# Kernel optimization log

Hardware: AMD Instinct MI355X
Metric: run time of the kernel (lower is better)

## Reference

```python
import jax, jax.numpy as jnp
import numpy as np

EPS = 1e-5  # torch LayerNorm default
H, DH = 8, 64  # heads, dim_head


def _ln(x, g, b):
    mu = jnp.mean(x, axis=-1, keepdims=True)
    var = jnp.var(x, axis=-1, keepdims=True)
    return (x - mu) / jnp.sqrt(var + EPS) * g + b


def setup_inputs() -> dict:
    key = jax.random.key(0)
    ks = jax.random.split(key, 8)
    B, N, M, D, CD = 4, 2048, 256, 1024, 768
    J = M + 1 + N  # context + null + self
    return {
        "x": jax.random.normal(ks[0], (B, N, D), jnp.float32),
        "context": jax.random.normal(ks[1], (B, M, CD), jnp.float32),
        "att_bias": jax.random.normal(ks[2], (B, H, N, J), jnp.float32) * 0.02,
        "ln_g": jnp.ones((D,), jnp.float32),
        "ln_b": jnp.zeros((D,), jnp.float32),
        "null_kv": jax.random.normal(ks[3], (2, DH), jnp.float32),
        "Wq": jax.random.normal(ks[4], (D, H * DH), jnp.float32) * 0.02,
        "Wkv": jax.random.normal(ks[5], (D, 2 * DH), jnp.float32) * 0.02,
        "cln_g": jnp.ones((CD,), jnp.float32),
        "cln_b": jnp.zeros((CD,), jnp.float32),
        "Wc": jax.random.normal(ks[6], (CD, 2 * DH), jnp.float32) * 0.02,
        "bc": jnp.zeros((2 * DH,), jnp.float32),
        "Wo": jax.random.normal(ks[7], (H * DH, D), jnp.float32) * 0.02,
        "oln_g": jnp.ones((D,), jnp.float32),
        "oln_b": jnp.zeros((D,), jnp.float32),
    }


def reference(x, context, att_bias, ln_g, ln_b, null_kv, Wq, Wkv,
              cln_g, cln_b, Wc, bc, Wo, oln_g, oln_b):
    B, N, D = x.shape
    scale = DH ** -0.5
    xn = _ln(x, ln_g, ln_b)
    # queries: per-head [b,h,n,dh], pre-scaled
    q = (xn @ Wq).reshape(B, N, H, DH).transpose(0, 2, 1, 3) * scale
    # shared single-head k/v [b,n,dh]
    kv = xn @ Wkv
    k, v = kv[..., :DH], kv[..., DH:]
    # context k/v [b,m,dh]
    ckv = _ln(context, cln_g, cln_b) @ Wc + bc
    ck, cv = ckv[..., :DH], ckv[..., DH:]
    # null kv token [b,1,dh]
    nk = jnp.broadcast_to(null_kv[0], (B, 1, DH))
    nv = jnp.broadcast_to(null_kv[1], (B, 1, DH))
    # torch order: cat null first, then context -> (ck, nk, k)
    k = jnp.concatenate([ck, nk, k], axis=1)  # [b, j, dh]
    v = jnp.concatenate([cv, nv, v], axis=1)
    score = jnp.einsum('bhid,bjd->bhij', q, k) + att_bias
    probs = jax.nn.softmax(score.astype(jnp.float32), axis=-1).astype(v.dtype)
    att = jnp.einsum('bhij,bjd->bhid', probs, v)
    att = att.transpose(0, 2, 1, 3).reshape(B, N, H * DH)
    return _ln(att @ Wo, oln_g, oln_b)
```

## Files before the change

kernel.cpp:

```cpp
#include <hip/hip_runtime.h>
#include <hip/hip_bf16.h>
#include <cstdint>
#include <cstddef>

#define Bq  4
#define Nq  2048
#define Mq  256
#define Dq  1024
#define CDq 768
#define Hq  8
#define DHq 64
#define Jq  2305
#define QKVN 640
#define NCH 37
#define J2  (NCH * 64)

typedef __bf16  bf16x8 __attribute__((ext_vector_type(8)));
typedef float   f32x4  __attribute__((ext_vector_type(4)));
typedef float   f32x4u __attribute__((ext_vector_type(4), aligned(4)));
typedef float   f32x16 __attribute__((ext_vector_type(16)));
typedef short   s16x8  __attribute__((ext_vector_type(8)));
typedef short   s16x4  __attribute__((ext_vector_type(4)));
typedef unsigned int u32x4 __attribute__((ext_vector_type(4)));
typedef unsigned short u16;
typedef unsigned int   u32;

__device__ __forceinline__ u16 f2b(float v) {
  unsigned x = __builtin_bit_cast(unsigned, v);
  unsigned r = (x + 0x7fffu + ((x >> 16) & 1u)) >> 16;
  return (u16)r;
}
__device__ __forceinline__ float b2f(u16 u) {
  unsigned x = ((unsigned)u) << 16;
  return __builtin_bit_cast(float, x);
}
__device__ __forceinline__ u32 cvtpk(float lo, float hi) {
  u32 r;
  asm("v_cvt_pk_bf16_f32 %0, %1, %2" : "=v"(r) : "v"(lo), "v"(hi));
  return r;
}
__device__ __forceinline__ void pswap(u32& a, u32& b) {
  asm volatile("v_permlane32_swap_b32 %0, %1" : "+v"(a), "+v"(b));
}
__device__ __forceinline__ f32x4 mfma16(bf16x8 a, bf16x8 b, f32x4 c) {
  return __builtin_amdgcn_mfma_f32_16x16x32_bf16(a, b, c, 0, 0, 0);
}
__device__ __forceinline__ f32x16 mfma32(bf16x8 a, bf16x8 b, f32x16 c) {
  return __builtin_amdgcn_mfma_f32_32x32x16_bf16(a, b, c, 0, 0, 0);
}
__device__ __forceinline__ bf16x8 frag_ld(const u16* p) {
  return __builtin_bit_cast(bf16x8, *(const s16x8*)p);
}
__device__ __forceinline__ void stout(float* p, float v) { *p = v; }
__device__ __forceinline__ void stout(u16*   p, float v) { *p = f2b(v); }

__device__ __forceinline__ void gl_lds16(const void* gSrc, void* ldsDst) {
  __builtin_amdgcn_global_load_lds(
      (const __attribute__((address_space(1))) void*)gSrc,
      (__attribute__((address_space(3))) void*)ldsDst, 16, 0, 0);
}

__global__ __launch_bounds__(256) void prep_kernel(
    const float* __restrict__ x,   const float* __restrict__ ln_g,
    const float* __restrict__ ln_b, u16* __restrict__ xn,
    const float* __restrict__ ctx, const float* __restrict__ cln_g,
    const float* __restrict__ cln_b, u16* __restrict__ ctxn,
    const float* __restrict__ Wq, const float* __restrict__ Wkv,
    const float* __restrict__ Wc, const float* __restrict__ Wo,
    u16* __restrict__ WqkvT, u16* __restrict__ WcT, u16* __restrict__ WoT) {
  const int tid = threadIdx.x;
  if (blockIdx.x < Bq * Nq + Bq * Mq) {
    const int row = blockIdx.x;
    const float* in; const float* g; const float* bb; u16* out; int D;
    if (row < Bq * Nq) {
      in = x + (size_t)row * Dq; g = ln_g; bb = ln_b;
      out = xn + (size_t)row * Dq; D = Dq;
    } else {
      int r2 = row - Bq * Nq;
      in = ctx + (size_t)r2 * CDq; g = cln_g; bb = cln_b;
      out = ctxn + (size_t)r2 * CDq; D = CDq;
    }
    __shared__ float buf[1024];
    __shared__ float red[8];
    float s = 0.f, s2 = 0.f;
    for (int i = tid; i < D; i += 256) {
      float v = in[i];
      buf[i] = v;
      s += v; s2 += v * v;
    }
    #pragma unroll
    for (int off = 32; off; off >>= 1) {
      s  += __shfl_down(s,  off);
      s2 += __shfl_down(s2, off);
    }
    if ((tid & 63) == 0) { red[tid >> 6] = s; red[4 + (tid >> 6)] = s2; }
    __syncthreads();
    float sum = red[0] + red[1] + red[2] + red[3];
    float sq  = red[4] + red[5] + red[6] + red[7];
    float mean = sum / D;
    float var  = sq / D - mean * mean;
    float rstd = rsqrtf(var + 1e-5f);
    for (int i = tid; i < D; i += 256)
      out[i] = f2b((buf[i] - mean) * rstd * g[i] + bb[i]);
  } else {
    __shared__ float T[32][33];
    int bid = blockIdx.x - (Bq * Nq + Bq * Mq);
    const float* W; u16* WT; int K, N, bx, by;
    if (bid < 512)      { W = Wq;  WT = WqkvT;                    K = 1024; N = 512;  bx = bid % 16;        by = bid / 16; }
    else if (bid < 640) { W = Wkv; WT = WqkvT + (size_t)512*1024; K = 1024; N = 128;  bx = (bid-512) % 4;   by = (bid-512) / 4; }
    else if (bid < 736) { W = Wc;  WT = WcT;                      K = 768;  N = 128;  bx = (bid-640) % 4;   by = (bid-640) / 4; }
    else                { W = Wo;  WT = WoT;                      K = 512;  N = 1024; bx = (bid-736) % 32;  by = (bid-736) / 32; }
    const int n0 = bx * 32, k0 = by * 32;
    const int tx = tid & 31, ty = tid >> 5;
    #pragma unroll
    for (int i = 0; i < 32; i += 8)
      T[ty + i][tx] = W[(size_t)(k0 + ty + i) * N + n0 + tx];
    __syncthreads();
    #pragma unroll
    for (int i = 0; i < 32; i += 8)
      WT[(size_t)(n0 + ty + i) * K + k0 + tx] = f2b(T[tx][ty + i]);
  }
}

template <typename OT>
__device__ __forceinline__ void gemm_body(const u16* __restrict__ A,
                                          const u16* __restrict__ BT,
                                          OT* __restrict__ C,
                                          int N, int K, int m0, int n0,
                                          u16* Al, u16* Bl) {
  const int tid  = threadIdx.x;
  const int lane = tid & 63, wave = tid >> 6;
  const int l16  = lane & 15, lhi = lane >> 4;
  const int wm = (wave >> 1) * 64, wn = (wave & 1) * 64;

  const int offB = (wave << 10) + (lane << 4);
  const int srow = offB >> 6;
  const int scby = offB & 63;

  f32x4 acc[4][4];
  #pragma unroll
  for (int i = 0; i < 4; ++i)
    #pragma unroll
    for (int j = 0; j < 4; ++j) acc[i][j] = f32x4{0.f, 0.f, 0.f, 0.f};

  for (int k0 = 0; k0 < K; k0 += 32) {
    __syncthreads();
    #pragma unroll
    for (int c = 0; c < 2; ++c) {
      gl_lds16((const char*)(A  + (size_t)(m0 + srow + c * 64) * K + k0) + scby,
               (char*)Al + c * 4096 + (wave << 10));
      gl_lds16((const char*)(BT + (size_t)(n0 + srow + c * 64) * K + k0) + scby,
               (char*)Bl + c * 4096 + (wave << 10));
    }
    __syncthreads();

    bf16x8 af[4], bfr[4];
    #pragma unroll
    for (int mt = 0; mt < 4; ++mt)
      af[mt] = frag_ld(Al + (wm + mt * 16 + l16) * 32 + lhi * 8);
    #pragma unroll
    for (int nt = 0; nt < 4; ++nt)
      bfr[nt] = frag_ld(Bl + (wn + nt * 16 + l16) * 32 + lhi * 8);
    __builtin_amdgcn_s_setprio(1);
    #pragma unroll
    for (int mt = 0; mt < 4; ++mt)
      #pragma unroll
      for (int nt = 0; nt < 4; ++nt)
        acc[mt][nt] = mfma16(af[mt], bfr[nt], acc[mt][nt]);
    __builtin_amdgcn_s_setprio(0);
  }

  #pragma unroll
  for (int mt = 0; mt < 4; ++mt)
    #pragma unroll
    for (int nt = 0; nt < 4; ++nt)
      #pragma unroll
      for (int r = 0; r < 4; ++r)
        stout(C + (size_t)(m0 + wm + mt * 16 + lhi * 4 + r) * N
                + (n0 + wn + nt * 16 + l16),
              acc[mt][nt][r]);
}

__global__ __launch_bounds__(256) void gemm_qkv_ckv(
    const u16* __restrict__ xn, const u16* __restrict__ WqkvT,
    u16* __restrict__ qkv,
    const u16* __restrict__ ctxn, const u16* __restrict__ WcT,
    u16* __restrict__ ckvb) {
  const u16 *A, *BT; u16* C; int N, K, m0, n0;
  if (blockIdx.y < 5) {
    A = xn; BT = WqkvT; C = qkv; N = QKVN; K = Dq;
    m0 = blockIdx.x * 128; n0 = blockIdx.y * 128;
  } else {
    if (blockIdx.x >= 8) return;
    A = ctxn; BT = WcT; C = ckvb; N = 2 * DHq; K = CDq;
    m0 = blockIdx.x * 128; n0 = 0;
  }
  __shared__ __align__(16) u16 Al[128 * 32];
  __shared__ __align__(16) u16 Bl[128 * 32];
  gemm_body<u16>(A, BT, C, N, K, m0, n0, Al, Bl);
}

__global__ void build_kv(const u16* __restrict__ qkv,
                         const u16* __restrict__ ckvb,
                         const float* __restrict__ nullkv,
                         const float* __restrict__ bc,
                         u16* __restrict__ Kt, u16* __restrict__ Vt) {
  int idx = blockIdx.x * 256 + threadIdx.x;
  if (idx >= Bq * J2 * 64) return;
  int d = idx & 63;
  int t = idx >> 6;
  int j = t % J2;
  int b = t / J2;
  float k = 0.f, v = 0.f;
  if (j < Mq) {
    const u16* p = ckvb + (size_t)(b * Mq + j) * 128;
    k = b2f(p[d])      + bc[d];
    v = b2f(p[64 + d]) + bc[64 + d];
  } else if (j == Mq) {
    k = nullkv[d];
    v = nullkv[64 + d];
  } else if (j < Jq) {
    const u16* p = qkv + (size_t)(b * Nq + (j - Mq - 1)) * QKVN + 512;
    k = b2f(p[d]);
    v = b2f(p[64 + d]);
  }
  int ch = j >> 6, row = j & 63;
  char* tbase = (char*)Kt + ((size_t)(b * NCH + ch)) * 8192;
  *(u16*)(tbase + row * 128 + ((d << 1) ^ ((row & 7) << 4))) = f2b(k);
  char* vbase = (char*)Vt + ((size_t)(b * NCH + ch)) * 8192;
  *(u16*)(vbase + d * 128 + ((row << 1) ^ ((d & 7) << 4))) = f2b(v);
}

__global__ __launch_bounds__(512) void attn_kernel(
    const u16* __restrict__ qkv, const u16* __restrict__ Kt,
    const u16* __restrict__ Vt, const float* __restrict__ bias,
    const u16* __restrict__ WoT, const float* __restrict__ oln_g,
    const float* __restrict__ oln_b, float* __restrict__ out) {
  __shared__ __align__(16) u16 Kl [2][4096];
  __shared__ __align__(16) u16 VTl[2][4096];
  __shared__ __align__(16) u16 attT[32][520];
  __shared__ float redS[8][32];
  __shared__ float redQ[8][32];
  const int tid  = threadIdx.x;
  const int wave = tid >> 6, lane = tid & 63;
  const int l = lane & 31, hi = lane >> 5;
  const int l16 = lane & 15, lhi = lane >> 4;
  const int qt = blockIdx.x, b = blockIdx.z;
  const int h = wave;
  const int qrow0 = qt * 32;

  bf16x8 qf[4];
  {
    const u16* qp = qkv + ((size_t)(b * Nq + qrow0 + l)) * QKVN
                        + h * DHq + hi * 8;
    #pragma unroll
    for (int kt = 0; kt < 4; ++kt) qf[kt] = frag_ld(qp + kt * 16);
  }

  float m_s = -INFINITY, l_s = 0.f;
  f32x16 oacc[2];
  #pragma unroll
  for (int dt = 0; dt < 2; ++dt)
    #pragma unroll
    for (int r = 0; r < 16; ++r) oacc[dt][r] = 0.f;

  const float* bp = bias
      + ((size_t)((b * Hq + h) * (size_t)Nq + qrow0 + l)) * Jq + 4 * hi;

  const size_t tb0 = (size_t)b * NCH;
  const int soff = (wave << 10) + (lane << 4);

  auto stage = [&](int buf, int ch) {
    const char* kt_ = (const char*)Kt + (tb0 + ch) * 8192 + soff;
    const char* vt_ = (const char*)Vt + (tb0 + ch) * 8192 + soff;
    gl_lds16(kt_, (char*)&Kl[buf][0]  + (wave << 10));
    gl_lds16(vt_, (char*)&VTl[buf][0] + (wave << 10));
  };

  auto loadBias = [&](f32x4 (&bv)[2][4], int ch) {
    const int jc = ch * 64;
    if (ch < NCH - 1) {
      #pragma unroll
      for (int jt = 0; jt < 2; ++jt)
        #pragma unroll
        for (int g = 0; g < 4; ++g)
          bv[jt][g] = (f32x4)(*(const f32x4u*)(bp + jc + jt * 32 + 8 * g));
    } else {
      #pragma unroll
      for (int jt = 0; jt < 2; ++jt)
        #pragma unroll
        for (int g = 0; g < 4; ++g)
          #pragma unroll
          for (int e = 0; e < 4; ++e) {
            int jg = jc + jt * 32 + 8 * g + 4 * hi + e;
            bv[jt][g][e] = (jg < Jq) ? bp[jc + jt * 32 + 8 * g + e] : -1e30f;
          }
    }
  };

  f32x4 bvA[2][4], bvB[2][4];
  stage(0, 0);
  loadBias(bvA, 0);
  __syncthreads();

  auto body = [&](int ch, f32x4 (&bvC)[2][4], f32x4 (&bvN)[2][4]) {
    const int cur = ch & 1;
    if (ch + 1 < NCH) {
      stage(cur ^ 1, ch + 1);
      loadBias(bvN, ch + 1);
    }
    const char* kbase = (const char*)&Kl[cur][0];
    const char* vbase = (const char*)&VTl[cur][0];

    f32x16 sacc[2];
    #pragma unroll
    for (int jt = 0; jt < 2; ++jt)
      #pragma unroll
      for (int r = 0; r < 16; ++r) sacc[jt][r] = 0.f;
    __builtin_amdgcn_s_setprio(1);
    #pragma unroll
    for (int jt = 0; jt < 2; ++jt) {
      const int row = jt * 32 + l;
      const int sw = (row & 7) << 4;
      #pragma unroll
      for (int kt = 0; kt < 4; ++kt) {
        bf16x8 kf = frag_ld((const u16*)(kbase + row * 128
                                         + ((kt * 32 + hi * 16) ^ sw)));
        sacc[jt] = mfma32(kf, qf[kt], sacc[jt]);
      }
    }
    __builtin_amdgcn_s_setprio(0);

    #pragma unroll
    for (int jt = 0; jt < 2; ++jt)
      #pragma unroll
      for (int r = 0; r < 16; ++r)
        sacc[jt][r] = sacc[jt][r] * 0.125f + bvC[jt][r >> 2][r & 3];

    float pmax = sacc[0][0];
    #pragma unroll
    for (int jt = 0; jt < 2; ++jt)
      #pragma unroll
      for (int r = 0; r < 16; ++r) pmax = fmaxf(pmax, sacc[jt][r]);
    pmax = fmaxf(pmax, __shfl_xor(pmax, 32));

    if (__any(pmax > m_s + 8.f)) {
      float mnew = fmaxf(m_s, pmax);
      float corr = __expf(m_s - mnew);
      l_s *= corr;
      m_s = mnew;
      #pragma unroll
      for (int r = 0; r < 16; ++r) {
        float c = __shfl(corr, (r & 3) + 8 * (r >> 2) + 4 * hi);
        oacc[0][r] *= c;
        oacc[1][r] *= c;
      }
    }

    float ps = 0.f;
    #pragma unroll
    for (int jt = 0; jt < 2; ++jt)
      #pragma unroll
      for (int r = 0; r < 16; ++r) {
        float pv = __expf(sacc[jt][r] - m_s);
        sacc[jt][r] = pv;
        ps += pv;
      }
    ps += __shfl_xor(ps, 32);
    l_s += ps;

    u32 pk[2][8];
    #pragma unroll
    for (int jt = 0; jt < 2; ++jt)
      #pragma unroll
      for (int g = 0; g < 4; ++g) {
        pk[jt][2 * g]     = cvtpk(sacc[jt][4 * g],     sacc[jt][4 * g + 1]);
        pk[jt][2 * g + 1] = cvtpk(sacc[jt][4 * g + 2], sacc[jt][4 * g + 3]);
      }

    #pragma unroll
    for (int kt = 0; kt < 4; ++kt) {
      const int t = kt & 1, js = kt >> 1;
      u32 a0 = pk[js][4 * t],     b0 = pk[js][4 * t + 2];
      u32 a1 = pk[js][4 * t + 1], b1 = pk[js][4 * t + 3];
      pswap(a0, b0);
      pswap(a1, b1);
      bf16x8 paf = __builtin_bit_cast(bf16x8, u32x4{a0, a1, b0, b1});
      __builtin_amdgcn_s_setprio(1);
      #pragma unroll
      for (int dt = 0; dt < 2; ++dt) {
        const int vrow = dt * 32 + l;
        bf16x8 vf = frag_ld((const u16*)(vbase + vrow * 128
                     + ((kt * 32 + hi * 16) ^ ((vrow & 7) << 4))));
        oacc[dt] = mfma32(paf, vf, oacc[dt]);
      }
      __builtin_amdgcn_s_setprio(0);
    }
    __syncthreads();
  };

  int ch = 0;
  while (true) {
    body(ch, bvA, bvB);
    if (++ch == NCH) break;
    body(ch, bvB, bvA);
    if (++ch == NCH) break;
  }

  {
    float linv = 1.0f / l_s;
    #pragma unroll
    for (int r = 0; r < 16; ++r) {
      const int qo = (r & 3) + 8 * (r >> 2) + 4 * hi;
      float inv = __shfl(linv, qo);
      attT[qo][h * 64 + l]      = f2b(oacc[0][r] * inv);
      attT[qo][h * 64 + 32 + l] = f2b(oacc[1][r] * inv);
    }
  }
  __syncthreads();

  const int n0w = wave * 128;
  f32x4 acc2[2][8];
  #pragma unroll
  for (int mt = 0; mt < 2; ++mt)
    #pragma unroll
    for (int nt = 0; nt < 8; ++nt) acc2[mt][nt] = f32x4{0.f, 0.f, 0.f, 0.f};

  for (int k0 = 0; k0 < 16; ++k0) {
    bf16x8 af[2];
    #pragma unroll
    for (int mt = 0; mt < 2; ++mt)
      af[mt] = frag_ld(&attT[mt * 16 + l16][k0 * 32 + lhi * 8]);
    __builtin_amdgcn_s_setprio(1);
    #pragma unroll
    for (int nt = 0; nt < 8; ++nt) {
      bf16x8 bfr = frag_ld(WoT + (size_t)(n0w + nt * 16 + l16) * 512
                               + k0 * 32 + lhi * 8);
      acc2[0][nt] = mfma16(af[0], bfr, acc2[0][nt]);
      acc2[1][nt] = mfma16(af[1], bfr, acc2[1][nt]);
    }
    __builtin_amdgcn_s_setprio(0);
  }

  float psum[8], psq[8];
  #pragma unroll
  for (int i = 0; i < 8; ++i) { psum[i] = 0.f; psq[i] = 0.f; }
  #pragma unroll
  for (int mt = 0; mt < 2; ++mt)
    #pragma unroll
    for (int nt = 0; nt < 8; ++nt)
      #pragma unroll
      for (int r = 0; r < 4; ++r) {
        float v = acc2[mt][nt][r];
        psum[mt * 4 + r] += v;
        psq[mt * 4 + r]  += v * v;
      }
  #pragma unroll
  for (int off = 1; off < 16; off <<= 1)
    #pragma unroll
    for (int i = 0; i < 8; ++i) {
      psum[i] += __shfl_xor(psum[i], off);
      psq[i]  += __shfl_xor(psq[i],  off);
    }
  if (l16 == 0) {
    #pragma unroll
    for (int mt = 0; mt < 2; ++mt)
      #pragma unroll
      for (int r = 0; r < 4; ++r) {
        redS[wave][mt * 16 + lhi * 4 + r] = psum[mt * 4 + r];
        redQ[wave][mt * 16 + lhi * 4 + r] = psq[mt * 4 + r];
      }
  }
  __syncthreads();

  float gv[8], bbv[8];
  #pragma unroll
  for (int nt = 0; nt < 8; ++nt) {
    gv[nt]  = oln_g[n0w + nt * 16 + l16];
    bbv[nt] = oln_b[n0w + nt * 16 + l16];
  }
  #pragma unroll
  for (int mt = 0; mt < 2; ++mt) {
    #pragma unroll
    for (int r = 0; r < 4; ++r) {
      const int row = mt * 16 + lhi * 4 + r;
      float s = 0.f, q2 = 0.f;
      #pragma unroll
      for (int w = 0; w < 8; ++w) { s += redS[w][row]; q2 += redQ[w][row]; }
      float mean = s * (1.0f / Dq);
      float var  = q2 * (1.0f / Dq) - mean * mean;
      float rstd = rsqrtf(var + 1e-5f);
      float* op = out + ((size_t)(b * Nq + qrow0 + row)) * Dq + n0w;
      #pragma unroll
      for (int nt = 0; nt < 8; ++nt)
        op[nt * 16 + l16] = (acc2[mt][nt][r] - mean) * rstd * gv[nt] + bbv[nt];
    }
  }
}

extern "C" void kernel_launch(void* const* d_in, const int* in_sizes, int n_in,
                              void* d_out, int out_size, void* d_ws, size_t ws_size,
                              hipStream_t stream) {
  const float* x       = (const float*)d_in[0];
  const float* context = (const float*)d_in[1];
  const float* att_bias= (const float*)d_in[2];
  const float* ln_g    = (const float*)d_in[3];
  const float* ln_b    = (const float*)d_in[4];
  const float* null_kv = (const float*)d_in[5];
  const float* Wq      = (const float*)d_in[6];
  const float* Wkv     = (const float*)d_in[7];
  const float* cln_g   = (const float*)d_in[8];
  const float* cln_b   = (const float*)d_in[9];
  const float* Wc      = (const float*)d_in[10];
  const float* bc      = (const float*)d_in[11];
  const float* Wo      = (const float*)d_in[12];
  const float* oln_g   = (const float*)d_in[13];
  const float* oln_b   = (const float*)d_in[14];
  float* out = (float*)d_out;

  char* p = (char*)d_ws;
  auto alloc = [&](size_t bytes) {
    void* r = (void*)p;
    p += (bytes + 255) & ~(size_t)255;
    return r;
  };
  u16* xn     = (u16*)alloc((size_t)Bq * Nq * Dq * 2);
  u16* ctxn   = (u16*)alloc((size_t)Bq * Mq * CDq * 2);
  u16* WqkvT  = (u16*)alloc((size_t)QKVN * Dq * 2);
  u16* WcT    = (u16*)alloc((size_t)2 * DHq * CDq * 2);
  u16* WoT    = (u16*)alloc((size_t)Dq * Hq * DHq * 2);
  u16* qkv    = (u16*)alloc((size_t)Bq * Nq * QKVN * 2);
  u16* ckvb   = (u16*)alloc((size_t)Bq * Mq * 2 * DHq * 2);
  u16* Ktil   = (u16*)alloc((size_t)Bq * NCH * 8192);
  u16* Vtil   = (u16*)alloc((size_t)Bq * NCH * 8192);

  prep_kernel<<<Bq * Nq + Bq * Mq + 1248, 256, 0, stream>>>(
      x, ln_g, ln_b, xn, context, cln_g, cln_b, ctxn,
      Wq, Wkv, Wc, Wo, WqkvT, WcT, WoT);

  gemm_qkv_ckv<<<dim3(Bq * Nq / 128, 6), 256, 0, stream>>>(
      xn, WqkvT, qkv, ctxn, WcT, ckvb);

  build_kv<<<(Bq * J2 * 64 + 255) / 256, 256, 0, stream>>>(
      qkv, ckvb, null_kv, bc, Ktil, Vtil);

  attn_kernel<<<dim3(Nq / 32, 1, Bq), 512, 0, stream>>>(
      qkv, Ktil, Vtil, att_bias, WoT, oln_g, oln_b, out);
}
```

Baseline: 249.4 us.

## Fuse K/V tile construction into projection GEMM epilogue, drop build_kv

The projection GEMM now writes the shared self K/V and the context K/V directly into the swizzled per-chunk K/V tile buffers, adding the context bias in its epilogue. This removes the intermediate kv columns from the qkv buffer and the separate build_kv pass that re-read them. A tiny fixup kernel writes the null token and zeroes the padding rows of the last chunk. The cost is scattered 2-byte epilogue stores, since V is written transposed.

```diff
diff --git a/kernel.cpp b/kernel.cpp
--- a/kernel.cpp
+++ b/kernel.cpp
@@ -11,7 +11,7 @@
 #define Hq  8
 #define DHq 64
 #define Jq  2305
-#define QKVN 640
+#define QSTR 512
 #define NCH 37
 #define J2  (NCH * 64)
 
@@ -20,7 +20,6 @@
 typedef float   f32x4u __attribute__((ext_vector_type(4), aligned(4)));
 typedef float   f32x16 __attribute__((ext_vector_type(16)));
 typedef short   s16x8  __attribute__((ext_vector_type(8)));
-typedef short   s16x4  __attribute__((ext_vector_type(4)));
 typedef unsigned int u32x4 __attribute__((ext_vector_type(4)));
 typedef unsigned short u16;
 typedef unsigned int   u32;
@@ -51,8 +50,6 @@
 __device__ __forceinline__ bf16x8 frag_ld(const u16* p) {
   return __builtin_bit_cast(bf16x8, *(const s16x8*)p);
 }
-__device__ __forceinline__ void stout(float* p, float v) { *p = v; }
-__device__ __forceinline__ void stout(u16*   p, float v) { *p = f2b(v); }
 
 __device__ __forceinline__ void gl_lds16(const void* gSrc, void* ldsDst) {
   __builtin_amdgcn_global_load_lds(
@@ -122,17 +119,29 @@
   }
 }
 
-template <typename OT>
-__device__ __forceinline__ void gemm_body(const u16* __restrict__ A,
-                                          const u16* __restrict__ BT,
-                                          OT* __restrict__ C,
-                                          int N, int K, int m0, int n0,
-                                          u16* Al, u16* Bl) {
+__global__ __launch_bounds__(256) void gemm_all(
+    const u16* __restrict__ xn, const u16* __restrict__ WqkvT,
+    u16* __restrict__ qkv,
+    const u16* __restrict__ ctxn, const u16* __restrict__ WcT,
+    const float* __restrict__ bc,
+    u16* __restrict__ Kt, u16* __restrict__ Vt) {
+  const int ymode = blockIdx.y;
+  const u16 *A, *BT; int K, m0, n0;
+  if (ymode < 5) {
+    A = xn; BT = WqkvT; K = Dq;
+    m0 = blockIdx.x * 128; n0 = ymode * 128;
+  } else {
+    if (blockIdx.x >= 8) return;
+    A = ctxn; BT = WcT; K = CDq;
+    m0 = blockIdx.x * 128; n0 = 0;
+  }
+  __shared__ __align__(16) u16 Al[128 * 32];
+  __shared__ __align__(16) u16 Bl[128 * 32];
+
   const int tid  = threadIdx.x;
   const int lane = tid & 63, wave = tid >> 6;
   const int l16  = lane & 15, lhi = lane >> 4;
   const int wm = (wave >> 1) * 64, wn = (wave & 1) * 64;
-
   const int offB = (wave << 10) + (lane << 4);
   const int srow = offB >> 6;
   const int scby = offB & 63;
@@ -170,65 +179,81 @@
     __builtin_amdgcn_s_setprio(0);
   }
 
-  #pragma unroll
-  for (int mt = 0; mt < 4; ++mt)
-    #pragma unroll
-    for (int nt = 0; nt < 4; ++nt)
-      #pragma unroll
-      for (int r = 0; r < 4; ++r)
-        stout(C + (size_t)(m0 + wm + mt * 16 + lhi * 4 + r) * N
-                + (n0 + wn + nt * 16 + l16),
-              acc[mt][nt][r]);
-}
-
-__global__ __launch_bounds__(256) void gemm_qkv_ckv(
-    const u16* __restrict__ xn, const u16* __restrict__ WqkvT,
-    u16* __restrict__ qkv,
-    const u16* __restrict__ ctxn, const u16* __restrict__ WcT,
-    u16* __restrict__ ckvb) {
-  const u16 *A, *BT; u16* C; int N, K, m0, n0;
-  if (blockIdx.y < 5) {
-    A = xn; BT = WqkvT; C = qkv; N = QKVN; K = Dq;
-    m0 = blockIdx.x * 128; n0 = blockIdx.y * 128;
+  if (ymode < 4) {
+    #pragma unroll
+    for (int mt = 0; mt < 4; ++mt)
+      #pragma unroll
+      for (int nt = 0; nt < 4; ++nt)
+        #pragma unroll
+        for (int r = 0; r < 4; ++r)
+          qkv[(size_t)(m0 + wm + mt * 16 + lhi * 4 + r) * QSTR
+              + n0 + wn + nt * 16 + l16] = f2b(acc[mt][nt][r]);
+  } else if (ymode == 4) {
+    #pragma unroll
+    for (int mt = 0; mt < 4; ++mt)
+      #pragma unroll
+      for (int r = 0; r < 4; ++r) {
+        const int rowg = m0 + wm + mt * 16 + lhi * 4 + r;
+        const int b = rowg >> 11;
+        const int j = (rowg & 2047) + Mq + 1;
+        const int ch = j >> 6, jr = j & 63;
+        char* kb = (char*)Kt + ((size_t)(b * NCH + ch)) * 8192;
+        char* vb = (char*)Vt + ((size_t)(b * NCH + ch)) * 8192;
+        #pragma unroll
+        for (int nt = 0; nt < 4; ++nt) {
+          const int d2 = wn + nt * 16 + l16;
+          const u16 val = f2b(acc[mt][nt][r]);
+          if (d2 < 64)
+            *(u16*)(kb + jr * 128 + ((d2 << 1) ^ ((jr & 7) << 4))) = val;
+          else {
+            const int d = d2 - 64;
+            *(u16*)(vb + d * 128 + ((jr << 1) ^ ((d & 7) << 4))) = val;
+          }
+        }
+      }
   } else {
-    if (blockIdx.x >= 8) return;
-    A = ctxn; BT = WcT; C = ckvb; N = 2 * DHq; K = CDq;
-    m0 = blockIdx.x * 128; n0 = 0;
-  }
-  __shared__ __align__(16) u16 Al[128 * 32];
-  __shared__ __align__(16) u16 Bl[128 * 32];
-  gemm_body<u16>(A, BT, C, N, K, m0, n0, Al, Bl);
-}
-
-__global__ void build_kv(const u16* __restrict__ qkv,
-                         const u16* __restrict__ ckvb,
-                         const float* __restrict__ nullkv,
-                         const float* __restrict__ bc,
-                         u16* __restrict__ Kt, u16* __restrict__ Vt) {
-  int idx = blockIdx.x * 256 + threadIdx.x;
-  if (idx >= Bq * J2 * 64) return;
-  int d = idx & 63;
-  int t = idx >> 6;
-  int j = t % J2;
-  int b = t / J2;
-  float k = 0.f, v = 0.f;
-  if (j < Mq) {
-    const u16* p = ckvb + (size_t)(b * Mq + j) * 128;
-    k = b2f(p[d])      + bc[d];
-    v = b2f(p[64 + d]) + bc[64 + d];
-  } else if (j == Mq) {
-    k = nullkv[d];
-    v = nullkv[64 + d];
-  } else if (j < Jq) {
-    const u16* p = qkv + (size_t)(b * Nq + (j - Mq - 1)) * QKVN + 512;
-    k = b2f(p[d]);
-    v = b2f(p[64 + d]);
-  }
-  int ch = j >> 6, row = j & 63;
-  char* tbase = (char*)Kt + ((size_t)(b * NCH + ch)) * 8192;
-  *(u16*)(tbase + row * 128 + ((d << 1) ^ ((row & 7) << 4))) = f2b(k);
-  char* vbase = (char*)Vt + ((size_t)(b * NCH + ch)) * 8192;
-  *(u16*)(vbase + d * 128 + ((row << 1) ^ ((d & 7) << 4))) = f2b(v);
+    #pragma unroll
+    for (int mt = 0; mt < 4; ++mt)
+      #pragma unroll
+      for (int r = 0; r < 4; ++r) {
+        const int rowg = m0 + wm + mt * 16 + lhi * 4 + r;
+        const int b = rowg >> 8;
+        const int j = rowg & 255;
+        const int ch = j >> 6, jr = j & 63;
+        char* kb = (char*)Kt + ((size_t)(b * NCH + ch)) * 8192;
+        char* vb = (char*)Vt + ((size_t)(b * NCH + ch)) * 8192;
+        #pragma unroll
+        for (int nt = 0; nt < 4; ++nt) {
+          const int d2 = wn + nt * 16 + l16;
+          const u16 val = f2b(acc[mt][nt][r] + bc[d2]);
+          if (d2 < 64)
+            *(u16*)(kb + jr * 128 + ((d2 << 1) ^ ((jr & 7) << 4))) = val;
+          else {
+            const int d = d2 - 64;
+            *(u16*)(vb + d * 128 + ((jr << 1) ^ ((d & 7) << 4))) = val;
+          }
+        }
+      }
+  }
+}
+
+__global__ __launch_bounds__(256) void kv_fixup(
+    const float* __restrict__ nullkv, u16* __restrict__ Kt,
+    u16* __restrict__ Vt) {
+  const int b = blockIdx.x, t = threadIdx.x;
+  char* kb4  = (char*)Kt + ((size_t)(b * NCH + 4))  * 8192;
+  char* vb4  = (char*)Vt + ((size_t)(b * NCH + 4))  * 8192;
+  char* kb36 = (char*)Kt + ((size_t)(b * NCH + 36)) * 8192;
+  char* vb36 = (char*)Vt + ((size_t)(b * NCH + 36)) * 8192;
+  if (t < 64) {
+    *(u16*)(kb4 + (t << 1)) = f2b(nullkv[t]);
+    *(u16*)(vb4 + t * 128 + ((t & 7) << 4)) = f2b(nullkv[64 + t]);
+  }
+  for (int idx = t; idx < 63 * 64; idx += 256) {
+    const int jr = 1 + (idx >> 6), d = idx & 63;
+    *(u16*)(kb36 + jr * 128 + ((d << 1) ^ ((jr & 7) << 4))) = 0;
+    *(u16*)(vb36 + d * 128 + ((jr << 1) ^ ((d & 7) << 4))) = 0;
+  }
 }
 
 __global__ __launch_bounds__(512) void attn_kernel(
@@ -251,7 +276,7 @@
 
   bf16x8 qf[4];
   {
-    const u16* qp = qkv + ((size_t)(b * Nq + qrow0 + l)) * QKVN
+    const u16* qp = qkv + ((size_t)(b * Nq + qrow0 + l)) * QSTR
                         + h * DHq + hi * 8;
     #pragma unroll
     for (int kt = 0; kt < 4; ++kt) qf[kt] = frag_ld(qp + kt * 16);
@@ -526,11 +551,10 @@
   };
   u16* xn     = (u16*)alloc((size_t)Bq * Nq * Dq * 2);
   u16* ctxn   = (u16*)alloc((size_t)Bq * Mq * CDq * 2);
-  u16* WqkvT  = (u16*)alloc((size_t)QKVN * Dq * 2);
+  u16* WqkvT  = (u16*)alloc((size_t)640 * Dq * 2);
   u16* WcT    = (u16*)alloc((size_t)2 * DHq * CDq * 2);
   u16* WoT    = (u16*)alloc((size_t)Dq * Hq * DHq * 2);
-  u16* qkv    = (u16*)alloc((size_t)Bq * Nq * QKVN * 2);
-  u16* ckvb   = (u16*)alloc((size_t)Bq * Mq * 2 * DHq * 2);
+  u16* qkv    = (u16*)alloc((size_t)Bq * Nq * QSTR * 2);
   u16* Ktil   = (u16*)alloc((size_t)Bq * NCH * 8192);
   u16* Vtil   = (u16*)alloc((size_t)Bq * NCH * 8192);
 
@@ -538,11 +562,10 @@
       x, ln_g, ln_b, xn, context, cln_g, cln_b, ctxn,
       Wq, Wkv, Wc, Wo, WqkvT, WcT, WoT);
 
-  gemm_qkv_ckv<<<dim3(Bq * Nq / 128, 6), 256, 0, stream>>>(
-      xn, WqkvT, qkv, ctxn, WcT, ckvb);
-
-  build_kv<<<(Bq * J2 * 64 + 255) / 256, 256, 0, stream>>>(
-      qkv, ckvb, null_kv, bc, Ktil, Vtil);
+  gemm_all<<<dim3(Bq * Nq / 128, 6), 256, 0, stream>>>(
+      xn, WqkvT, qkv, ctxn, WcT, bc, Ktil, Vtil);
+
+  kv_fixup<<<Bq, 256, 0, stream>>>(null_kv, Ktil, Vtil);
 
   attn_kernel<<<dim3(Nq / 32, 1, Bq), 512, 0, stream>>>(
       qkv, Ktil, Vtil, att_bias, WoT, oln_g, oln_b, out);
```

Measured after the change: 248.9 us. About the same (-0.2%).
